# Kernel optimization log

Hardware: AMD Instinct MI355X
Metric: run time of the kernel (lower is better)

## Reference

```python
import jax, jax.numpy as jnp
import numpy as np

TEMPERATURE = 0.07
NORMALIZE = True
NEG_INF = -1e30


def setup_inputs() -> dict:
    key = jax.random.key(0)
    features = jax.random.normal(key, (8192, 512), dtype=jnp.float32)
    return {"features": features}


def reference(features):
    # features: [B, D]
    B = features.shape[0]
    if NORMALIZE:
        norm = jnp.linalg.norm(features, axis=1, keepdims=True)
        features = features / jnp.maximum(norm, 1e-12)
    # [B, B] similarity matrix
    sim = jnp.matmul(features, features.T) / TEMPERATURE

    # default SimCLR labels: arange(B//2) repeated twice -> pair (i, i + B//2)
    half = jnp.arange(B // 2, dtype=jnp.int32)
    labels = jnp.concatenate([half, half])
    eq = labels[None, :] == labels[:, None]          # [B, B]
    diag = jnp.eye(B, dtype=bool)
    mask_pos = eq & ~diag                            # positives per row

    # Original per-row CE: logits = cat(pos_sims, neg_sims) (= all j != i),
    # target index 0 = FIRST positive (lowest column index). Loss_i =
    # logsumexp_{j != i}(sim[i, j]) - sim[i, first_pos_i].
    sim_masked = jnp.where(diag, NEG_INF, sim)
    lse = jax.scipy.special.logsumexp(sim_masked, axis=1)   # [B]

    first_pos = jnp.argmax(mask_pos, axis=1)                 # first True per row
    pos_sim = jnp.take_along_axis(sim, first_pos[:, None], axis=1)[:, 0]

    has_pos = jnp.any(mask_pos, axis=1)
    losses = jnp.where(has_pos, lse - pos_sim, 0.0)
    count = jnp.maximum(jnp.sum(has_pos.astype(jnp.float32)), 1.0)
    return jnp.sum(losses) / count
```

## Files before the change

### kernel.cpp

```cpp
#include <hip/hip_runtime.h>
#include <hip/hip_bf16.h>
#include <stdint.h>

#define BATCH 8192
#define DIM   512
#define BM    256
#define NT    (BATCH / BM)
#define NPAIR (NT * (NT + 1) / 2)
#define NBLK  (NPAIR * 2)

#define FEAT_SCALE 4.5398164f
#define LN2        0.69314718055994531f

typedef __attribute__((ext_vector_type(8))) short short8;
typedef __attribute__((ext_vector_type(4))) float f32x4;

__device__ __forceinline__ void gld_lds16(const void* g, void* l) {
  __builtin_amdgcn_global_load_lds(
      (__attribute__((address_space(1))) void*)(uintptr_t)g,
      (__attribute__((address_space(3))) void*)(uintptr_t)l,
      16, 0, 0);
}

__global__ __launch_bounds__(256) void normalize_bf16(
    const float* __restrict__ x, __hip_bfloat16* __restrict__ o,
    float* __restrict__ rowsum) {
  const int wv = threadIdx.x >> 6, lane = threadIdx.x & 63;
  const int row = blockIdx.x * 4 + wv;
  if (lane == 0) rowsum[row] = 0.0f;
  const float4* xr = (const float4*)(x + (size_t)row * DIM);
  const float4 v0 = xr[lane];
  const float4 v1 = xr[lane + 64];
  float ss = v0.x * v0.x + v0.y * v0.y + v0.z * v0.z + v0.w * v0.w +
             v1.x * v1.x + v1.y * v1.y + v1.z * v1.z + v1.w * v1.w;
#pragma unroll
  for (int m = 32; m > 0; m >>= 1) ss += __shfl_xor(ss, m, 64);
  const float inv = FEAT_SCALE / fmaxf(sqrtf(ss), 1e-12f);
  ushort4 p0, p1;
  p0.x = __bfloat16_as_ushort(__float2bfloat16(v0.x * inv));
  p0.y = __bfloat16_as_ushort(__float2bfloat16(v0.y * inv));
  p0.z = __bfloat16_as_ushort(__float2bfloat16(v0.z * inv));
  p0.w = __bfloat16_as_ushort(__float2bfloat16(v0.w * inv));
  p1.x = __bfloat16_as_ushort(__float2bfloat16(v1.x * inv));
  p1.y = __bfloat16_as_ushort(__float2bfloat16(v1.y * inv));
  p1.z = __bfloat16_as_ushort(__float2bfloat16(v1.z * inv));
  p1.w = __bfloat16_as_ushort(__float2bfloat16(v1.w * inv));
  ushort4* orow = (ushort4*)(o + (size_t)row * DIM);
  orow[lane]      = p0;
  orow[lane + 64] = p1;
}

__global__ __launch_bounds__(512, 2) void sim_lse_kernel(
    const __hip_bfloat16* __restrict__ F, float* __restrict__ rowsum,
    float* __restrict__ possim) {
  extern __shared__ char smem[];
  float* colAcc = (float*)(smem + 98304);

  const int t  = blockIdx.x;
  const int pr = t >> 1;
  const int hb = t & 1;
  int by = (int)((65.0f - sqrtf(65.0f * 65.0f - 8.0f * (float)pr)) * 0.5f);
  if (by > NT - 1) by = NT - 1;
  if (by < 0) by = 0;
  while ((by + 1) * (65 - (by + 1)) / 2 <= pr) ++by;
  while (by * (65 - by) / 2 > pr) --by;
  const int bx = by + (pr - by * (65 - by) / 2);
  const bool diagTile = (bx == by);
  const bool hasPos = (bx == by + NT / 2);

  const int rowB = by * BM + hb * 128;
  const int colB = bx * BM;

  const int tid  = threadIdx.x;
  const int lane = tid & 63;
  const int wv   = tid >> 6;
  const int q    = lane >> 4;
  const int l15  = lane & 15;
  const int waveM = wv >> 2;
  const int waveN = wv & 3;

  const int rs = tid >> 2, ss = tid & 3;
  const int sw = ss ^ ((rs >> 1) & 3);
  const __hip_bfloat16* gA  = F + (size_t)(rowB + rs) * DIM + sw * 8;
  const __hip_bfloat16* gB0 = F + (size_t)(colB + rs) * DIM + sw * 8;
  const __hip_bfloat16* gB1 = gB0 + (size_t)128 * DIM;

  const int swz  = (q ^ ((l15 >> 1) & 3)) * 16;
  const int aoff = (waveM * 64 + l15) * 64 + swz;
  const int boff = (waveN * 64 + l15) * 64 + swz;

  if (tid < 256) colAcc[tid] = 0.0f;

  f32x4 acc[4][4] = {};
  short8 a[4], b[4];

#define STAGE(T_, KK_) do {                                                   \
    const int ko_ = ((T_) & 7) * 64 + (KK_) * 32;                             \
    const int pb_ = ((T_) & 1) * 2 + (KK_);                                   \
    gld_lds16(gA  + ko_, smem + pb_ * 8192 + wv * 1024);                      \
    gld_lds16(gB0 + ko_, smem + 32768 + pb_ * 16384 + wv * 1024);             \
    gld_lds16(gB1 + ko_, smem + 32768 + pb_ * 16384 + 8192 + wv * 1024);      \
  } while (0)

#define PHASE(TB_, KK_, ST_, SKK_) do {                                       \
    const char* pa_ = smem + ((TB_) * 2 + (KK_)) * 8192 + aoff;               \
    a[0] = *(const short8*)(pa_);                                             \
    a[1] = *(const short8*)(pa_ + 1024);                                      \
    a[2] = *(const short8*)(pa_ + 2048);                                      \
    a[3] = *(const short8*)(pa_ + 3072);                                      \
    const char* pb_ = smem + 32768 + ((TB_) * 2 + (KK_)) * 16384 + boff;      \
    b[0] = *(const short8*)(pb_);                                             \
    b[1] = *(const short8*)(pb_ + 1024);                                      \
    b[2] = *(const short8*)(pb_ + 2048);                                      \
    b[3] = *(const short8*)(pb_ + 3072);                                      \
    STAGE(ST_, SKK_);                                                         \
    asm volatile("s_waitcnt vmcnt(6)" ::: "memory");                          \
    __builtin_amdgcn_s_barrier();                                             \
    __builtin_amdgcn_s_setprio(1);                                            \
    _Pragma("unroll")                                                         \
    for (int m_ = 0; m_ < 4; ++m_)                                            \
      _Pragma("unroll")                                                       \
      for (int n_ = 0; n_ < 4; ++n_)                                          \
        acc[m_][n_] = __builtin_amdgcn_mfma_f32_16x16x32_bf16(                \
            a[m_], b[n_], acc[m_][n_], 0, 0, 0);                              \
    __builtin_amdgcn_s_setprio(0);                                            \
    __builtin_amdgcn_s_barrier();                                             \
  } while (0)

  STAGE(0, 0); STAGE(0, 1); STAGE(1, 0);
  asm volatile("s_waitcnt vmcnt(3)" ::: "memory");
  __builtin_amdgcn_s_barrier();

#pragma unroll
  for (int T = 0; T < 8; ++T) {
    PHASE(T & 1, 0, T + 1, 1);
    PHASE(T & 1, 1, T + 2, 0);
  }

  asm volatile("s_waitcnt vmcnt(0)" ::: "memory");
  __builtin_amdgcn_s_barrier();

  float* redBuf = (float*)smem;
  float cp[4] = {0.f, 0.f, 0.f, 0.f};
  f32x4 rp[4];

#pragma unroll
  for (int mi = 0; mi < 4; ++mi) {
    f32x4 r = {0.f, 0.f, 0.f, 0.f};
#pragma unroll
    for (int ni = 0; ni < 4; ++ni) {
      const int lc = waveN * 64 + ni * 16 + l15;
#pragma unroll
      for (int rr = 0; rr < 4; ++rr) {
        const int lr = waveM * 64 + mi * 16 + q * 4 + rr;
        const float s = acc[mi][ni][rr];
        float e = exp2f(s);
        if (diagTile && lc == hb * 128 + lr) e = 0.0f;
        r[rr] += e;
        cp[ni] += e;
        if (hasPos && lc == hb * 128 + lr) {
          const int gi = rowB + lr;
          possim[gi] = s;
          possim[gi + BATCH / 2] = s;
        }
      }
    }
    rp[mi] = r;
  }

  {
    float* wb = redBuf + (waveN * 16 + l15) * 132 + waveM * 64 + q * 4;
#pragma unroll
    for (int mi = 0; mi < 4; ++mi) *(f32x4*)(wb + mi * 16) = rp[mi];
  }

  if (!diagTile) {
#pragma unroll
    for (int ni = 0; ni < 4; ++ni) {
      float c = cp[ni];
      c += __shfl_xor(c, 16, 64);
      c += __shfl_xor(c, 32, 64);
      if (q == 0) atomicAdd(&colAcc[waveN * 64 + ni * 16 + l15], c);
    }
  }
  asm volatile("s_waitcnt lgkmcnt(0)" ::: "memory");
  __builtin_amdgcn_s_barrier();

  {
    const int row = tid >> 2, g = tid & 3;
    const float* bp = redBuf + g * 132 + row;
    float s = 0.f;
#pragma unroll
    for (int j = 0; j < 16; ++j) s += bp[j * 528];
    s += __shfl_xor(s, 1, 64);
    s += __shfl_xor(s, 2, 64);
    if (g == 0) atomicAdd(&rowsum[rowB + row], s);
  }
  if (!diagTile && tid < 256)
    atomicAdd(&rowsum[colB + tid], colAcc[tid]);
}

__global__ __launch_bounds__(1024) void finalize_kernel(
    const float* __restrict__ rowsum, const float* __restrict__ possim,
    float* __restrict__ out) {
  float acc = 0.0f;
  for (int i = threadIdx.x; i < BATCH; i += 1024)
    acc += __logf(rowsum[i]) - possim[i] * LN2;
#pragma unroll
  for (int m = 32; m > 0; m >>= 1) acc += __shfl_xor(acc, m, 64);
  __shared__ float ws[16];
  const int lane = threadIdx.x & 63, wv = threadIdx.x >> 6;
  if (lane == 0) ws[wv] = acc;
  __syncthreads();
  if (threadIdx.x == 0) {
    float tot = 0.0f;
#pragma unroll
    for (int k = 0; k < 16; ++k) tot += ws[k];
    out[0] = tot * (1.0f / (float)BATCH);
  }
}

extern "C" void kernel_launch(void* const* d_in, const int* in_sizes, int n_in,
                              void* d_out, int out_size, void* d_ws, size_t ws_size,
                              hipStream_t stream) {
  const float* x = (const float*)d_in[0];
  float* out = (float*)d_out;

  __hip_bfloat16* Fb = (__hip_bfloat16*)d_ws;
  float* rowsum = (float*)((char*)d_ws + (size_t)BATCH * DIM * sizeof(__hip_bfloat16));
  float* possim = rowsum + BATCH;

  static bool attr_done = false;
  if (!attr_done) {
    (void)hipFuncSetAttribute(reinterpret_cast<const void*>(sim_lse_kernel),
                              hipFuncAttributeMaxDynamicSharedMemorySize, 99328);
    attr_done = true;
  }

  normalize_bf16<<<BATCH / 4, 256, 0, stream>>>(x, Fb, rowsum);
  sim_lse_kernel<<<NBLK, 512, 99328, stream>>>(Fb, rowsum, possim);
  finalize_kernel<<<1, 1024, 0, stream>>>(rowsum, possim, out);
}
```

Before: 128.4 us.

## Use full 256x256 output tiles per block with a restructured LDS pipeline

```diff
diff --git a/kernel.cpp b/kernel.cpp
--- a/kernel.cpp
+++ b/kernel.cpp
@@ -7,7 +7,6 @@
 #define BM    256
 #define NT    (BATCH / BM)
 #define NPAIR (NT * (NT + 1) / 2)
-#define NBLK  (NPAIR * 2)
 
 #define FEAT_SCALE 4.5398164f
 #define LN2        0.69314718055994531f
@@ -54,11 +53,9 @@
     const __hip_bfloat16* __restrict__ F, float* __restrict__ rowsum,
     float* __restrict__ possim) {
   extern __shared__ char smem[];
-  float* colAcc = (float*)(smem + 98304);
-
-  const int t  = blockIdx.x;
-  const int pr = t >> 1;
-  const int hb = t & 1;
+  float* colAcc = (float*)(smem + 131072);
+
+  const int pr = blockIdx.x;
   int by = (int)((65.0f - sqrtf(65.0f * 65.0f - 8.0f * (float)pr)) * 0.5f);
   if (by > NT - 1) by = NT - 1;
   if (by < 0) by = 0;
@@ -68,7 +65,7 @@
   const bool diagTile = (bx == by);
   const bool hasPos = (bx == by + NT / 2);
 
-  const int rowB = by * BM + hb * 128;
+  const int rowB = by * BM;
   const int colB = bx * BM;
 
   const int tid  = threadIdx.x;
@@ -79,89 +76,106 @@
   const int waveM = wv >> 2;
   const int waveN = wv & 3;
 
-  const int rs = tid >> 2, ss = tid & 3;
-  const int sw = ss ^ ((rs >> 1) & 3);
-  const __hip_bfloat16* gA  = F + (size_t)(rowB + rs) * DIM + sw * 8;
-  const __hip_bfloat16* gB0 = F + (size_t)(colB + rs) * DIM + sw * 8;
-  const __hip_bfloat16* gB1 = gB0 + (size_t)128 * DIM;
-
-  const int swz  = (q ^ ((l15 >> 1) & 3)) * 16;
-  const int aoff = (waveM * 64 + l15) * 64 + swz;
-  const int boff = (waveN * 64 + l15) * 64 + swz;
-
-  if (tid < 256) colAcc[tid] = 0.0f;
-
-  f32x4 acc[4][4] = {};
+  const int r0 = tid >> 3, c0 = tid & 7;
+  const int csrc = c0 ^ (r0 & 7);
+  const __hip_bfloat16* gAp = F + (size_t)(rowB + r0) * DIM + csrc * 8;
+  const __hip_bfloat16* gBp = F + (size_t)(colB + r0) * DIM + csrc * 8;
+
+#define STAGE_A(Tn) do {                                                      \
+    const int kk_ = ((Tn) & 7) * 64;                                          \
+    char* d_ = smem + ((Tn) & 1) * 65536 + wv * 1024;                         \
+    gld_lds16(gAp + kk_,                 d_);                                 \
+    gld_lds16(gAp + kk_ + 32768,         d_ + 8192);                          \
+    gld_lds16(gAp + kk_ + 65536,         d_ + 16384);                         \
+    gld_lds16(gAp + kk_ + 98304,         d_ + 24576);                         \
+  } while (0)
+#define STAGE_B(Tn) do {                                                      \
+    const int kk_ = ((Tn) & 7) * 64;                                          \
+    char* d_ = smem + ((Tn) & 1) * 65536 + 32768 + wv * 1024;                 \
+    gld_lds16(gBp + kk_,                 d_);                                 \
+    gld_lds16(gBp + kk_ + 32768,         d_ + 8192);                          \
+    gld_lds16(gBp + kk_ + 65536,         d_ + 16384);                         \
+    gld_lds16(gBp + kk_ + 98304,         d_ + 24576);                         \
+  } while (0)
+
+  const int cs0 = ((q)     ^ (l15 & 7)) * 16;
+  const int cs1 = ((4 + q) ^ (l15 & 7)) * 16;
+  const int abase = waveM * 16384 + l15 * 128;
+  const int bbase = 32768 + (waveN >> 1) * 16384 + ((waveN & 1) * 64 + l15) * 128;
+
   short8 a[4], b[4];
-
-#define STAGE(T_, KK_) do {                                                   \
-    const int ko_ = ((T_) & 7) * 64 + (KK_) * 32;                             \
-    const int pb_ = ((T_) & 1) * 2 + (KK_);                                   \
-    gld_lds16(gA  + ko_, smem + pb_ * 8192 + wv * 1024);                      \
-    gld_lds16(gB0 + ko_, smem + 32768 + pb_ * 16384 + wv * 1024);             \
-    gld_lds16(gB1 + ko_, smem + 32768 + pb_ * 16384 + 8192 + wv * 1024);      \
-  } while (0)
-
-#define PHASE(TB_, KK_, ST_, SKK_) do {                                       \
-    const char* pa_ = smem + ((TB_) * 2 + (KK_)) * 8192 + aoff;               \
-    a[0] = *(const short8*)(pa_);                                             \
-    a[1] = *(const short8*)(pa_ + 1024);                                      \
-    a[2] = *(const short8*)(pa_ + 2048);                                      \
-    a[3] = *(const short8*)(pa_ + 3072);                                      \
-    const char* pb_ = smem + 32768 + ((TB_) * 2 + (KK_)) * 16384 + boff;      \
-    b[0] = *(const short8*)(pb_);                                             \
-    b[1] = *(const short8*)(pb_ + 1024);                                      \
-    b[2] = *(const short8*)(pb_ + 2048);                                      \
-    b[3] = *(const short8*)(pb_ + 3072);                                      \
-    STAGE(ST_, SKK_);                                                         \
-    asm volatile("s_waitcnt vmcnt(6)" ::: "memory");                          \
-    __builtin_amdgcn_s_barrier();                                             \
+  f32x4 acc[8][4] = {};
+
+#define RD_B(BF_, CS_) do {                                                   \
+    const char* p_ = smem + (BF_) * 65536 + bbase + (CS_);                    \
+    b[0] = *(const short8*)(p_);                                              \
+    b[1] = *(const short8*)(p_ + 2048);                                       \
+    b[2] = *(const short8*)(p_ + 4096);                                       \
+    b[3] = *(const short8*)(p_ + 6144);                                       \
+  } while (0)
+#define RD_A(BF_, LH_, CS_) do {                                              \
+    const char* p_ = smem + (BF_) * 65536 + abase + (LH_) * 8192 + (CS_);     \
+    a[0] = *(const short8*)(p_);                                              \
+    a[1] = *(const short8*)(p_ + 2048);                                       \
+    a[2] = *(const short8*)(p_ + 4096);                                       \
+    a[3] = *(const short8*)(p_ + 6144);                                       \
+  } while (0)
+#define MFMA16(LH_) do {                                                      \
     __builtin_amdgcn_s_setprio(1);                                            \
     _Pragma("unroll")                                                         \
     for (int m_ = 0; m_ < 4; ++m_)                                            \
       _Pragma("unroll")                                                       \
       for (int n_ = 0; n_ < 4; ++n_)                                          \
-        acc[m_][n_] = __builtin_amdgcn_mfma_f32_16x16x32_bf16(                \
-            a[m_], b[n_], acc[m_][n_], 0, 0, 0);                              \
+        acc[(LH_) * 4 + m_][n_] = __builtin_amdgcn_mfma_f32_16x16x32_bf16(    \
+            a[m_], b[n_], acc[(LH_) * 4 + m_][n_], 0, 0, 0);                  \
     __builtin_amdgcn_s_setprio(0);                                            \
-    __builtin_amdgcn_s_barrier();                                             \
-  } while (0)
-
-  STAGE(0, 0); STAGE(0, 1); STAGE(1, 0);
-  asm volatile("s_waitcnt vmcnt(3)" ::: "memory");
-  __builtin_amdgcn_s_barrier();
-
-#pragma unroll
-  for (int T = 0; T < 8; ++T) {
-    PHASE(T & 1, 0, T + 1, 1);
-    PHASE(T & 1, 1, T + 2, 0);
-  }
-
+    __builtin_amdgcn_sched_barrier(0);                                        \
+  } while (0)
+
+  if (tid < 256) colAcc[tid] = 0.0f;
+
+  STAGE_A(0); STAGE_B(0);
   asm volatile("s_waitcnt vmcnt(0)" ::: "memory");
   __builtin_amdgcn_s_barrier();
 
+#pragma unroll
+  for (int T = 0; T < 8; ++T) {
+    const int bf = T & 1;
+    RD_B(bf, cs0); RD_A(bf, 0, cs0);
+    if (T < 7) STAGE_A(T + 1);
+    MFMA16(0);
+    RD_A(bf, 1, cs0);
+    if (T < 7) STAGE_B(T + 1);
+    MFMA16(1);
+    RD_B(bf, cs1); RD_A(bf, 0, cs1);
+    MFMA16(0);
+    RD_A(bf, 1, cs1);
+    MFMA16(1);
+    asm volatile("s_waitcnt vmcnt(0)" ::: "memory");
+    __builtin_amdgcn_s_barrier();
+  }
+
   float* redBuf = (float*)smem;
   float cp[4] = {0.f, 0.f, 0.f, 0.f};
-  f32x4 rp[4];
-
-#pragma unroll
-  for (int mi = 0; mi < 4; ++mi) {
+  f32x4 rp[8];
+
+#pragma unroll
+  for (int mi = 0; mi < 8; ++mi) {
     f32x4 r = {0.f, 0.f, 0.f, 0.f};
 #pragma unroll
     for (int ni = 0; ni < 4; ++ni) {
       const int lc = waveN * 64 + ni * 16 + l15;
 #pragma unroll
       for (int rr = 0; rr < 4; ++rr) {
-        const int lr = waveM * 64 + mi * 16 + q * 4 + rr;
+        const int lr = waveM * 128 + mi * 16 + q * 4 + rr;
         const float s = acc[mi][ni][rr];
         float e = exp2f(s);
-        if (diagTile && lc == hb * 128 + lr) e = 0.0f;
+        if (diagTile && lc == lr) e = 0.0f;
         r[rr] += e;
         cp[ni] += e;
-        if (hasPos && lc == hb * 128 + lr) {
-          const int gi = rowB + lr;
-          possim[gi] = s;
-          possim[gi + BATCH / 2] = s;
+        if (hasPos && lc == lr) {
+          possim[rowB + lr] = s;
+          possim[rowB + lr + BATCH / 2] = s;
         }
       }
     }
@@ -169,9 +183,9 @@
   }
 
   {
-    float* wb = redBuf + (waveN * 16 + l15) * 132 + waveM * 64 + q * 4;
-#pragma unroll
-    for (int mi = 0; mi < 4; ++mi) *(f32x4*)(wb + mi * 16) = rp[mi];
+    float* wb = redBuf + (waveN * 16 + l15) * 260 + waveM * 128 + q * 4;
+#pragma unroll
+    for (int mi = 0; mi < 8; ++mi) *(f32x4*)(wb + mi * 16) = rp[mi];
   }
 
   if (!diagTile) {
@@ -187,14 +201,13 @@
   __builtin_amdgcn_s_barrier();
 
   {
-    const int row = tid >> 2, g = tid & 3;
-    const float* bp = redBuf + g * 132 + row;
-    float s = 0.f;
-#pragma unroll
-    for (int j = 0; j < 16; ++j) s += bp[j * 528];
-    s += __shfl_xor(s, 1, 64);
-    s += __shfl_xor(s, 2, 64);
-    if (g == 0) atomicAdd(&rowsum[rowB + row], s);
+    const int row = tid >> 1, half = tid & 1;
+    const float* bp = redBuf + half * 32 * 260 + row;
+    float ssum = 0.f;
+#pragma unroll
+    for (int j = 0; j < 32; ++j) ssum += bp[j * 260];
+    ssum += __shfl_xor(ssum, 1, 64);
+    if (half == 0) atomicAdd(&rowsum[rowB + row], ssum);
   }
   if (!diagTile && tid < 256)
     atomicAdd(&rowsum[colB + tid], colAcc[tid]);
@@ -233,11 +246,11 @@
   static bool attr_done = false;
   if (!attr_done) {
     (void)hipFuncSetAttribute(reinterpret_cast<const void*>(sim_lse_kernel),
-                              hipFuncAttributeMaxDynamicSharedMemorySize, 99328);
+                              hipFuncAttributeMaxDynamicSharedMemorySize, 132096);
     attr_done = true;
   }
 
   normalize_bf16<<<BATCH / 4, 256, 0, stream>>>(x, Fb, rowsum);
-  sim_lse_kernel<<<NBLK, 512, 99328, stream>>>(Fb, rowsum, possim);
+  sim_lse_kernel<<<NPAIR, 512, 132096, stream>>>(Fb, rowsum, possim);
   finalize_kernel<<<1, 1024, 0, stream>>>(rowsum, possim, out);
 }
```

Result: faster. 120.5 us (-6.1%).

## Switch GEMM mainloop to triple-buffered 64-wide K tiles with 8-way swizzle

Applied to the files above, without the earlier changes.

```diff
diff --git a/kernel.cpp b/kernel.cpp
--- a/kernel.cpp
+++ b/kernel.cpp
@@ -54,7 +54,7 @@
     const __hip_bfloat16* __restrict__ F, float* __restrict__ rowsum,
     float* __restrict__ possim) {
   extern __shared__ char smem[];
-  float* colAcc = (float*)(smem + 98304);
+  float* colAcc = (float*)(smem + 147456);
 
   const int t  = blockIdx.x;
   const int pr = t >> 1;
@@ -79,43 +79,48 @@
   const int waveM = wv >> 2;
   const int waveN = wv & 3;
 
-  const int rs = tid >> 2, ss = tid & 3;
-  const int sw = ss ^ ((rs >> 1) & 3);
-  const __hip_bfloat16* gA  = F + (size_t)(rowB + rs) * DIM + sw * 8;
-  const __hip_bfloat16* gB0 = F + (size_t)(colB + rs) * DIM + sw * 8;
-  const __hip_bfloat16* gB1 = gB0 + (size_t)128 * DIM;
-
-  const int swz  = (q ^ ((l15 >> 1) & 3)) * 16;
-  const int aoff = (waveM * 64 + l15) * 64 + swz;
-  const int boff = (waveN * 64 + l15) * 64 + swz;
-
-  if (tid < 256) colAcc[tid] = 0.0f;
-
+  const int r0 = tid >> 3, c0 = tid & 7;
+  const int csrc = c0 ^ (r0 & 7);
+  const __hip_bfloat16* gAp = F + (size_t)(rowB + r0) * DIM + csrc * 8;
+  const __hip_bfloat16* gBp = F + (size_t)(colB + r0) * DIM + csrc * 8;
+
+#define STAGE_FH(Tn) do {                                                     \
+    const int ko_ = ((Tn) & 7) * 64;                                          \
+    const int pA_ = ((Tn) % 3) * 16384;                                       \
+    const int pB_ = 49152 + ((Tn) % 3) * 32768;                               \
+    gld_lds16(gAp + ko_,             smem + pA_ + wv * 1024);                 \
+    gld_lds16(gAp + ko_ + 64 * DIM,  smem + pA_ + 8192 + wv * 1024);          \
+    gld_lds16(gBp + ko_,             smem + pB_ + wv * 1024);                 \
+  } while (0)
+#define STAGE_SH(Tn) do {                                                     \
+    const int ko_ = ((Tn) & 7) * 64;                                          \
+    const int pB_ = 49152 + ((Tn) % 3) * 32768;                               \
+    gld_lds16(gBp + ko_ + 64 * DIM,  smem + pB_ + 8192 + wv * 1024);          \
+    gld_lds16(gBp + ko_ + 128 * DIM, smem + pB_ + 16384 + wv * 1024);         \
+    gld_lds16(gBp + ko_ + 192 * DIM, smem + pB_ + 24576 + wv * 1024);         \
+  } while (0)
+
+  const int cs0 = ((q)     ^ (l15 & 7)) * 16;
+  const int cs1 = ((4 + q) ^ (l15 & 7)) * 16;
+  const int arow = waveM * 8192 + l15 * 128;
+  const int brow = waveN * 8192 + l15 * 128;
+
+  short8 a[4], b[4];
   f32x4 acc[4][4] = {};
-  short8 a[4], b[4];
-
-#define STAGE(T_, KK_) do {                                                   \
-    const int ko_ = ((T_) & 7) * 64 + (KK_) * 32;                             \
-    const int pb_ = ((T_) & 1) * 2 + (KK_);                                   \
-    gld_lds16(gA  + ko_, smem + pb_ * 8192 + wv * 1024);                      \
-    gld_lds16(gB0 + ko_, smem + 32768 + pb_ * 16384 + wv * 1024);             \
-    gld_lds16(gB1 + ko_, smem + 32768 + pb_ * 16384 + 8192 + wv * 1024);      \
-  } while (0)
-
-#define PHASE(TB_, KK_, ST_, SKK_) do {                                       \
-    const char* pa_ = smem + ((TB_) * 2 + (KK_)) * 8192 + aoff;               \
+
+#define RD(PL_, CS_) do {                                                     \
+    const char* pa_ = smem + (PL_) * 16384 + arow + (CS_);                    \
     a[0] = *(const short8*)(pa_);                                             \
-    a[1] = *(const short8*)(pa_ + 1024);                                      \
-    a[2] = *(const short8*)(pa_ + 2048);                                      \
-    a[3] = *(const short8*)(pa_ + 3072);                                      \
-    const char* pb_ = smem + 32768 + ((TB_) * 2 + (KK_)) * 16384 + boff;      \
+    a[1] = *(const short8*)(pa_ + 2048);                                      \
+    a[2] = *(const short8*)(pa_ + 4096);                                      \
+    a[3] = *(const short8*)(pa_ + 6144);                                      \
+    const char* pb_ = smem + 49152 + (PL_) * 32768 + brow + (CS_);            \
     b[0] = *(const short8*)(pb_);                                             \
-    b[1] = *(const short8*)(pb_ + 1024);                                      \
-    b[2] = *(const short8*)(pb_ + 2048);                                      \
-    b[3] = *(const short8*)(pb_ + 3072);                                      \
-    STAGE(ST_, SKK_);                                                         \
-    asm volatile("s_waitcnt vmcnt(6)" ::: "memory");                          \
-    __builtin_amdgcn_s_barrier();                                             \
+    b[1] = *(const short8*)(pb_ + 2048);                                      \
+    b[2] = *(const short8*)(pb_ + 4096);                                      \
+    b[3] = *(const short8*)(pb_ + 6144);                                      \
+  } while (0)
+#define MFMA16() do {                                                         \
     __builtin_amdgcn_s_setprio(1);                                            \
     _Pragma("unroll")                                                         \
     for (int m_ = 0; m_ < 4; ++m_)                                            \
@@ -124,17 +129,30 @@
         acc[m_][n_] = __builtin_amdgcn_mfma_f32_16x16x32_bf16(                \
             a[m_], b[n_], acc[m_][n_], 0, 0, 0);                              \
     __builtin_amdgcn_s_setprio(0);                                            \
-    __builtin_amdgcn_s_barrier();                                             \
-  } while (0)
-
-  STAGE(0, 0); STAGE(0, 1); STAGE(1, 0);
-  asm volatile("s_waitcnt vmcnt(3)" ::: "memory");
+  } while (0)
+
+  if (tid < 256) colAcc[tid] = 0.0f;
+
+  STAGE_FH(0); STAGE_SH(0); STAGE_FH(1); STAGE_SH(1);
+  asm volatile("s_waitcnt vmcnt(6)" ::: "memory");
   __builtin_amdgcn_s_barrier();
 
 #pragma unroll
   for (int T = 0; T < 8; ++T) {
-    PHASE(T & 1, 0, T + 1, 1);
-    PHASE(T & 1, 1, T + 2, 0);
+    const int pl = T % 3;
+    RD(pl, cs0);
+    STAGE_FH(T + 2);
+    __builtin_amdgcn_s_barrier();
+    asm volatile("s_waitcnt lgkmcnt(0)" ::: "memory");
+    MFMA16();
+    __builtin_amdgcn_s_barrier();
+    RD(pl, cs1);
+    STAGE_SH(T + 2);
+    asm volatile("s_waitcnt vmcnt(6)" ::: "memory");
+    __builtin_amdgcn_s_barrier();
+    asm volatile("s_waitcnt lgkmcnt(0)" ::: "memory");
+    MFMA16();
+    __builtin_amdgcn_s_barrier();
   }
 
   asm volatile("s_waitcnt vmcnt(0)" ::: "memory");
@@ -159,9 +177,8 @@
         r[rr] += e;
         cp[ni] += e;
         if (hasPos && lc == hb * 128 + lr) {
-          const int gi = rowB + lr;
-          possim[gi] = s;
-          possim[gi + BATCH / 2] = s;
+          possim[rowB + lr] = s;
+          possim[rowB + lr + BATCH / 2] = s;
         }
       }
     }
@@ -188,10 +205,9 @@
 
   {
     const int row = tid >> 2, g = tid & 3;
-    const float* bp = redBuf + g * 132 + row;
     float s = 0.f;
 #pragma unroll
-    for (int j = 0; j < 16; ++j) s += bp[j * 528];
+    for (int j = 0; j < 16; ++j) s += redBuf[(g * 16 + j) * 132 + row];
     s += __shfl_xor(s, 1, 64);
     s += __shfl_xor(s, 2, 64);
     if (g == 0) atomicAdd(&rowsum[rowB + row], s);
@@ -233,11 +249,11 @@
   static bool attr_done = false;
   if (!attr_done) {
     (void)hipFuncSetAttribute(reinterpret_cast<const void*>(sim_lse_kernel),
-                              hipFuncAttributeMaxDynamicSharedMemorySize, 99328);
+                              hipFuncAttributeMaxDynamicSharedMemorySize, 148480);
     attr_done = true;
   }
 
   normalize_bf16<<<BATCH / 4, 256, 0, stream>>>(x, Fb, rowsum);
-  sim_lse_kernel<<<NBLK, 512, 99328, stream>>>(Fb, rowsum, possim);
+  sim_lse_kernel<<<NBLK, 512, 148480, stream>>>(Fb, rowsum, possim);
   finalize_kernel<<<1, 1024, 0, stream>>>(rowsum, possim, out);
 }
```

Result: no change. 128.3 us (-0.1%).
